# Optimization experiments

Hardware: AMD Instinct MI355X
Metric: run time of the kernel (lower is better)

Reference implementation:

```python
import jax, jax.numpy as jnp
import numpy as np

AX = (-2, -1)
LAMBDA = 0.05
ITERS = 6

# torch fft_2d_img  = fftshift(ifft2(ifftshift(x)))  (used in the FORWARD model)
# torch ifft_2d_img = ifftshift(fft2(fftshift(x)))   (used in the ADJOINT model)

def _fwd_xform(x):
    return jnp.fft.fftshift(jnp.fft.ifft2(jnp.fft.ifftshift(x, axes=AX), axes=AX, norm='ortho'), axes=AX)

def _adj_xform(x):
    return jnp.fft.ifftshift(jnp.fft.fft2(jnp.fft.fftshift(x, axes=AX), axes=AX, norm='ortho'), axes=AX)

def _forward_model(img, S, mask):
    # img [b,t,h,w] -> masked multicoil k-space [b,t,c,h,w]
    return mask * _fwd_xform(S * img[:, :, None])

def _adjoint_model(k, S):
    # k [b,t,c,h,w] -> coil-combined image [b,t,h,w]
    return jnp.sum(jnp.conj(S) * _adj_xform(k), axis=2)

def _system_matrix_R(p, S, L, mask):
    # p [b,sv,h,w]; L [b,t,sv]
    expanded = jnp.einsum('bts,bshw->bthw', L, p)
    combined = _adjoint_model(_forward_model(expanded, S, mask), S)
    out = jnp.einsum('bts,bthw->bshw', jnp.conj(L), combined)
    return out + LAMBDA * p

def _cg_solve(b_vec, S, L, mask):
    z0 = jnp.zeros_like(b_vec)
    rs0 = jnp.vdot(b_vec, b_vec)

    def step(carry, _):
        z, r, p, rs_old, done = carry
        Ap = _system_matrix_R(p, S, L, mask)
        alpha = rs_old / (jnp.vdot(p, Ap) + 1e-20)
        z_n = z + alpha * p
        r_n = r - alpha * Ap
        rs_new = jnp.vdot(r_n, r_n)
        p_n = r_n + (rs_new / (rs_old + 1e-20)) * p
        # replicate torch early-break: freeze state once residual is tiny
        z_o = jnp.where(done, z, z_n)
        r_o = jnp.where(done, r, r_n)
        p_o = jnp.where(done, p, p_n)
        rs_o = jnp.where(done, rs_old, rs_new)
        done_n = done | (jnp.abs(rs_o) < 1e-10)
        return (z_o, r_o, p_o, rs_o, done_n), None

    carry0 = (z0, b_vec, b_vec, rs0, jnp.array(False))
    (z, _, _, _, _), _ = jax.lax.scan(step, carry0, None, length=ITERS)
    return z

def setup_inputs() -> dict:
    key = jax.random.key(0)
    ks = jax.random.split(key, 9)
    b, t, c, h, w, sv = 2, 12, 10, 256, 256, 3
    f32 = jnp.float32
    inp = {
        'k_real': jax.random.normal(ks[0], (b, t, c, h, w), f32),
        'k_imag': jax.random.normal(ks[1], (b, t, c, h, w), f32),
        'mo_real': jax.random.normal(ks[2], (b, sv, h, w), f32),
        'mo_imag': jax.random.normal(ks[3], (b, sv, h, w), f32),
        's_real': jax.random.normal(ks[4], (b, 1, c, h, w), f32),
        's_imag': jax.random.normal(ks[5], (b, 1, c, h, w), f32),
        'tb_real': jax.random.normal(ks[6], (b, t, sv), f32),
        'tb_imag': jax.random.normal(ks[7], (b, t, sv), f32),
        'mask': (jax.random.uniform(ks[8], (b, t, 1, h, w)) < 0.35).astype(f32),
    }
    return inp

def reference(k_real, k_imag, mo_real, mo_imag, s_real, s_imag, tb_real, tb_imag, mask):
    Y = k_real + 1j * k_imag          # [b,t,c,h,w]
    MO = mo_real + 1j * mo_imag       # [b,sv,h,w]
    S = s_real + 1j * s_imag          # [b,1,c,h,w]
    L = tb_real + 1j * tb_imag        # [b,t,sv]
    # b = L^H A^H Y + lambda * model_output
    b_vec = jnp.einsum('bts,bthw->bshw', jnp.conj(L), _adjoint_model(Y, S)) + LAMBDA * MO
    z = _cg_solve(b_vec, S, L, mask)  # [b,sv,h,w] complex
    return jnp.stack([z.real, z.imag], axis=-1)  # [b,sv,h,w,2] float32
```

## Files before the change

kernel.cpp:

```cpp
#include <hip/hip_runtime.h>
#include <math.h>

#define HW 65536
#define LAM 0.05f

struct Scal {
  double pap_re, pap_im, rs_acc, rs_old;
  int done, cnt;
};

__device__ __forceinline__ float2 cadd(float2 a, float2 b){ return make_float2(a.x+b.x, a.y+b.y); }
__device__ __forceinline__ float2 csub(float2 a, float2 b){ return make_float2(a.x-b.x, a.y-b.y); }
__device__ __forceinline__ float2 cmul(float2 a, float2 b){
  return make_float2(a.x*b.x - a.y*b.y, a.x*b.y + a.y*b.x);
}
__device__ __forceinline__ float2 cmulj(float2 a, float2 b){
  return make_float2(a.x*b.x + a.y*b.y, a.x*b.y - a.y*b.x);
}
__device__ __forceinline__ int rev4(int p){
  return ((p&3)<<6) | (((p>>2)&3)<<4) | (((p>>4)&3)<<2) | ((p>>6)&3);
}
__device__ __forceinline__ int swz(int p){ return p ^ (p>>4); }

__device__ __forceinline__ void wave_lds_sync(){
  __builtin_amdgcn_wave_barrier();
  __asm__ __volatile__("s_waitcnt lgkmcnt(0)" ::: "memory");
  __builtin_amdgcn_wave_barrier();
}

template<int SIGN>
__device__ void wave_fft256w(float2* buf, int lane){
#pragma unroll
  for (int st=0; st<4; ++st){
    const int B = 256 >> (2*st);
    const int Q = B >> 2;
    int m   = lane & (Q-1);
    int blk = lane >> (6 - 2*st);
    int p0  = blk*B + m;
    float2 x0 = buf[swz(p0      )];
    float2 x1 = buf[swz(p0 +   Q)];
    float2 x2 = buf[swz(p0 + 2*Q)];
    float2 x3 = buf[swz(p0 + 3*Q)];
    float2 a  = cadd(x0,x2), bm = csub(x0,x2);
    float2 c  = cadd(x1,x3), d  = csub(x1,x3);
    float2 jd = make_float2(-(float)SIGN*d.y, (float)SIGN*d.x);
    float2 y0 = cadd(a,c);
    float2 y2 = csub(a,c);
    float2 y1 = cadd(bm,jd);
    float2 y3 = csub(bm,jd);
    if (st < 3){
      float ang = (float)SIGN * 6.28318530717958647f * (float)m / (float)B;
      float s1, c1;
      __sincosf(ang, &s1, &c1);
      float2 w1 = make_float2(c1, s1);
      float2 w2 = make_float2(c1*c1 - s1*s1, 2.f*c1*s1);
      float2 w3 = cmul(w1, w2);
      y1 = cmul(y1, w1); y2 = cmul(y2, w2); y3 = cmul(y3, w3);
      buf[swz(p0      )] = y0;
      buf[swz(p0 +   Q)] = y1;
      buf[swz(p0 + 2*Q)] = y2;
      buf[swz(p0 + 3*Q)] = y3;
    } else {
      buf[swz(rev4(4*lane+0))] = y0;
      buf[swz(rev4(4*lane+1))] = y1;
      buf[swz(rev4(4*lane+2))] = y2;
      buf[swz(rev4(4*lane+3))] = y3;
    }
    wave_lds_sync();
  }
}

__global__ __launch_bounds__(256) void k_w(const float* __restrict__ mask,
                                           const float* __restrict__ tbr,
                                           const float* __restrict__ tbi,
                                           float2* __restrict__ Wb,
                                           Scal* sc){
  if (blockIdx.x==0 && blockIdx.y==0 && threadIdx.x==0){
    sc->pap_re=0.0; sc->pap_im=0.0; sc->rs_acc=0.0; sc->rs_old=0.0;
    sc->done=0; sc->cnt=0;
  }
  __shared__ float2 wt[9][16][17];
  int tid = threadIdx.x;
  int bx = blockIdx.x;
  int b  = blockIdx.y;
  int u0 = (bx>>4)<<4, v0 = (bx&15)<<4;
  int u_l = tid>>4, v_l = tid&15;
  int pix = (u0+u_l)*256 + (v0+v_l);
  float d0=0,d1=0,d2=0, o01r=0,o01i=0, o02r=0,o02i=0, o12r=0,o12i=0;
#pragma unroll
  for (int t=0;t<12;t++){
    float m = mask[(size_t)(b*12+t)*HW + pix];
    int lb = (b*12+t)*3;
    float l0r = tbr[lb+0], l0i = tbi[lb+0];
    float l1r = tbr[lb+1], l1i = tbi[lb+1];
    float l2r = tbr[lb+2], l2i = tbi[lb+2];
    d0 += m*(l0r*l0r + l0i*l0i);
    d1 += m*(l1r*l1r + l1i*l1i);
    d2 += m*(l2r*l2r + l2i*l2i);
    o01r += m*(l0r*l1r + l0i*l1i); o01i += m*(l0r*l1i - l0i*l1r);
    o02r += m*(l0r*l2r + l0i*l2i); o02i += m*(l0r*l2i - l0i*l2r);
    o12r += m*(l1r*l2r + l1i*l2i); o12i += m*(l1r*l2i - l1i*l2r);
  }
  const float s = 1.0f/65536.0f;
  wt[0][u_l][v_l] = make_float2(d0*s, 0.f);
  wt[1][u_l][v_l] = make_float2(o01r*s,  o01i*s);
  wt[2][u_l][v_l] = make_float2(o02r*s,  o02i*s);
  wt[3][u_l][v_l] = make_float2(o01r*s, -o01i*s);
  wt[4][u_l][v_l] = make_float2(d1*s, 0.f);
  wt[5][u_l][v_l] = make_float2(o12r*s,  o12i*s);
  wt[6][u_l][v_l] = make_float2(o02r*s, -o02i*s);
  wt[7][u_l][v_l] = make_float2(o12r*s, -o12i*s);
  wt[8][u_l][v_l] = make_float2(d2*s, 0.f);
  __syncthreads();
  int u_l2 = tid&15, v_l2 = tid>>4;
#pragma unroll
  for (int k=0;k<9;k++){
    Wb[ ((size_t)(b*9+k)*256 + (v0+v_l2))*256 + (u0+u_l2) ] = wt[k][u_l2][v_l2];
  }
}

__global__ __launch_bounds__(256) void k_yhat(const float* __restrict__ kr,
                                              const float* __restrict__ ki,
                                              const float* __restrict__ tbr,
                                              const float* __restrict__ tbi,
                                              float2* __restrict__ bufA){
  int tid = threadIdx.x;
  int pr  = blockIdx.x*256 + tid;
  int pix = pr*2;
  int c = blockIdx.y, b = blockIdx.z;
  float aer[3]={0,0,0}, aei[3]={0,0,0}, bor[3]={0,0,0}, boi[3]={0,0,0};
#pragma unroll
  for (int t=0;t<12;t++){
    size_t off = ((size_t)((b*12+t)*10+c))*HW + pix;
    float2 yr = *(const float2*)(kr+off);
    float2 yi = *(const float2*)(ki+off);
    int lb = (b*12+t)*3;
#pragma unroll
    for (int s=0;s<3;s++){
      float lr = tbr[lb+s], li = tbi[lb+s];
      aer[s] += lr*yr.x + li*yi.x;  aei[s] += lr*yi.x - li*yr.x;
      bor[s] += lr*yr.y + li*yi.y;  boi[s] += lr*yi.y - li*yr.y;
    }
  }
  float sg0 = (((pix>>8) ^ pix) & 1) ? -1.f : 1.f;
  float s0 = sg0*(1.0f/256.0f), s1 = -s0;
  size_t base = ((size_t)(b*10+c))*3*HW + pix;
#pragma unroll
  for (int s=0;s<3;s++){
    float4 o = make_float4(aer[s]*s0, aei[s]*s0, bor[s]*s1, boi[s]*s1);
    *(float4*)(&bufA[base + (size_t)s*HW]) = o;
  }
}

template<int MODE>
__global__ __launch_bounds__(256) void k_colpass(float2* __restrict__ bufA,
                                                 const float2* __restrict__ Wb){
  __shared__ float2 lb[24*257];
  int tid = threadIdx.x, wave = tid>>6, lane = tid&63;
  int j0 = blockIdx.x*8;
  int c = blockIdx.y, b = blockIdx.z;
  for (int s=0;s<3;s++){
    const float2* src = bufA + ((size_t)(b*30 + c*3 + s))*HW;
#pragma unroll
    for (int it=0; it<8; it++){
      int idx = it*256 + tid;
      int u = idx>>3, col = idx&7;
      lb[(s*8+col)*257 + swz(u)] = src[u*256 + j0 + col];
    }
  }
  __syncthreads();
  if (MODE==0){
    for (int fc=wave; fc<24; fc+=4)
      wave_fft256w<-1>(&lb[fc*257], lane);
  } else {
    for (int fc=wave; fc<24; fc+=4)
      wave_fft256w<1>(&lb[fc*257], lane);
    const float2* Wp = Wb + (size_t)b*9*HW;
#pragma unroll
    for (int cc=0; cc<2; cc++){
      int col = wave + 4*cc;
      int v = j0 + col;
#pragma unroll
      for (int it=0; it<4; it++){
        int u = lane + it*64;
        int su = swz(u);
        float2 x0 = lb[(0*8+col)*257 + su];
        float2 x1 = lb[(1*8+col)*257 + su];
        float2 x2 = lb[(2*8+col)*257 + su];
        size_t wb = (size_t)v*256 + u;
        float2 y0 = cmul(Wp[(size_t)0*HW + wb], x0);
        y0 = cadd(y0, cmul(Wp[(size_t)1*HW + wb], x1));
        y0 = cadd(y0, cmul(Wp[(size_t)2*HW + wb], x2));
        float2 y1 = cmul(Wp[(size_t)3*HW + wb], x0);
        y1 = cadd(y1, cmul(Wp[(size_t)4*HW + wb], x1));
        y1 = cadd(y1, cmul(Wp[(size_t)5*HW + wb], x2));
        float2 y2 = cmul(Wp[(size_t)6*HW + wb], x0);
        y2 = cadd(y2, cmul(Wp[(size_t)7*HW + wb], x1));
        y2 = cadd(y2, cmul(Wp[(size_t)8*HW + wb], x2));
        lb[(0*8+col)*257 + su] = y0;
        lb[(1*8+col)*257 + su] = y1;
        lb[(2*8+col)*257 + su] = y2;
      }
    }
    wave_lds_sync();
    for (int fc=wave; fc<24; fc+=4)
      wave_fft256w<-1>(&lb[fc*257], lane);
  }
  __syncthreads();
  for (int s=0;s<3;s++){
    float2* dst = bufA + ((size_t)(b*30 + c*3 + s))*HW;
#pragma unroll
    for (int it=0; it<8; it++){
      int idx = it*256 + tid;
      int u = idx>>3, col = idx&7;
      dst[u*256 + j0 + col] = lb[(s*8+col)*257 + swz(u)];
    }
  }
}

__global__ __launch_bounds__(256) void k_spfft(const float2* __restrict__ p,
                                               const float* __restrict__ sr_,
                                               const float* __restrict__ si_,
                                               float2* __restrict__ bufA){
  __shared__ float2 lb[30*257];
  int tid = threadIdx.x, wave = tid>>6, lane = tid&63;
  int r = blockIdx.x, b = blockIdx.y;
  int k = tid;
  float2 pv[3];
#pragma unroll
  for (int s=0;s<3;s++)
    pv[s] = p[(size_t)(b*3+s)*HW + (size_t)r*256 + k];
  int sk = swz(k);
#pragma unroll
  for (int c=0;c<10;c++){
    size_t so = (size_t)(b*10+c)*HW + (size_t)r*256 + k;
    float2 sv = make_float2(sr_[so], si_[so]);
#pragma unroll
    for (int s=0;s<3;s++)
      lb[(c*3+s)*257 + sk] = cmul(sv, pv[s]);
  }
  __syncthreads();
  for (int pl=wave; pl<30; pl+=4){
    float2* lw = &lb[pl*257];
    wave_fft256w<1>(lw, lane);
    float2* dst = bufA + (size_t)(b*30+pl)*HW + (size_t)r*256;
#pragma unroll
    for (int q=0;q<4;q++){
      int kk = lane + 64*q;
      dst[kk] = lw[swz(kk)];
    }
  }
}

template<int SETUP>
__global__ __launch_bounds__(256) void k_rowcomb(const float2* __restrict__ bufA,
                                                 const float* __restrict__ sr_,
                                                 const float* __restrict__ si_,
                                                 const float* __restrict__ mor,
                                                 const float* __restrict__ moi,
                                                 const float2* __restrict__ pad,
                                                 float2* __restrict__ out,
                                                 Scal* sc){
  __shared__ float2 lb[30*257];
  __shared__ double sd[4], sd2[4];
  int tid = threadIdx.x, wave = tid>>6, lane = tid&63;
  int r = blockIdx.x, b = blockIdx.y;
  if (!SETUP && r==0 && b==0 && tid==0) sc->rs_acc = 0.0;
  for (int pl=wave; pl<30; pl+=4){
    const float2* src = bufA + (size_t)(b*30+pl)*HW + (size_t)r*256;
    float2* lw = &lb[pl*257];
#pragma unroll
    for (int q=0;q<4;q++){
      int kk = lane + 64*q;
      lw[swz(kk)] = src[kk];
    }
    wave_lds_sync();
    wave_fft256w<-1>(lw, lane);
  }
  __syncthreads();
  int k = tid, sk = swz(k);
  float2 a0 = make_float2(0,0), a1 = make_float2(0,0), a2 = make_float2(0,0);
#pragma unroll
  for (int c=0;c<10;c++){
    size_t so = (size_t)(b*10+c)*HW + (size_t)r*256 + k;
    float2 sv = make_float2(sr_[so], si_[so]);
    a0 = cadd(a0, cmulj(sv, lb[(c*3+0)*257 + sk]));
    a1 = cadd(a1, cmulj(sv, lb[(c*3+1)*257 + sk]));
    a2 = cadd(a2, cmulj(sv, lb[(c*3+2)*257 + sk]));
  }
  float2 accs[3] = {a0, a1, a2};
  double dre = 0.0, dim = 0.0;
#pragma unroll
  for (int s=0;s<3;s++){
    size_t oi = (size_t)(b*3+s)*HW + (size_t)r*256 + k;
    float2 acc = accs[s];
    if (SETUP){
      float sg = ((r ^ k) & 1) ? -1.f : 1.f;
      float sl = sg * LAM;
      acc.x += sl*mor[oi]; acc.y += sl*moi[oi];
      out[oi] = acc;
      dre += (double)acc.x*acc.x + (double)acc.y*acc.y;
    } else {
      float2 av = pad[oi];
      acc.x += LAM*av.x; acc.y += LAM*av.y;
      out[oi] = acc;
      dre += (double)av.x*acc.x + (double)av.y*acc.y;
      dim += (double)av.x*acc.y - (double)av.y*acc.x;
    }
  }
  for (int off=32; off>0; off>>=1){
    dre += __shfl_down(dre, off, 64);
    if (!SETUP) dim += __shfl_down(dim, off, 64);
  }
  if (lane==0){ sd[wave] = dre; sd2[wave] = dim; }
  __syncthreads();
  if (tid==0){
    double tre = sd[0]+sd[1]+sd[2]+sd[3];
    if (SETUP){
      atomicAdd(&sc->rs_acc, tre);
    } else {
      double tim = sd2[0]+sd2[1]+sd2[2]+sd2[3];
      atomicAdd(&sc->pap_re, tre);
      atomicAdd(&sc->pap_im, tim);
    }
  }
}

__global__ __launch_bounds__(256) void k_cginit(const float2* __restrict__ bvec,
                                                float2* __restrict__ z,
                                                float2* __restrict__ r,
                                                float2* __restrict__ p,
                                                Scal* sc){
  int i = blockIdx.x*256 + threadIdx.x;
  float2 bv = bvec[i];
  z[i] = make_float2(0.f,0.f);
  r[i] = bv; p[i] = bv;
  if (i==0){ sc->rs_old = sc->rs_acc; sc->pap_re=0.0; sc->pap_im=0.0; }
}

__global__ __launch_bounds__(256) void k_upzr(float2* __restrict__ z,
                                              float2* __restrict__ r,
                                              const float2* __restrict__ p,
                                              const float2* __restrict__ Ap,
                                              Scal* sc){
  __shared__ double sd[4];
  int tid = threadIdx.x;
  int i = blockIdx.x*256 + tid;
  int done = sc->done;
  double local = 0.0;
  if (!done){
    double dre = sc->pap_re + 1e-20, dim = sc->pap_im;
    double den = dre*dre + dim*dim;
    double rs = sc->rs_old;
    float2 alpha = make_float2((float)( rs*dre/den), (float)(-rs*dim/den));
    float2 pv = p[i], apv = Ap[i];
    float2 zv = cadd(z[i], cmul(alpha, pv));
    float2 rv = csub(r[i], cmul(alpha, apv));
    z[i] = zv; r[i] = rv;
    local = (double)rv.x*rv.x + (double)rv.y*rv.y;
  }
  for (int off=32; off>0; off>>=1) local += __shfl_down(local, off, 64);
  if ((tid&63)==0) sd[tid>>6] = local;
  __syncthreads();
  if (tid==0 && !done){
    atomicAdd(&sc->rs_acc, sd[0]+sd[1]+sd[2]+sd[3]);
  }
}

__global__ __launch_bounds__(256) void k_upp(float2* __restrict__ p,
                                             const float2* __restrict__ r,
                                             Scal* sc){
  __shared__ int amLast;
  int tid = threadIdx.x;
  int i = blockIdx.x*256 + tid;
  int done = sc->done;
  if (!done){
    float beta = (float)(sc->rs_acc / (sc->rs_old + 1e-20));
    float2 pv = p[i];
    p[i] = make_float2(r[i].x + beta*pv.x, r[i].y + beta*pv.y);
  }
  if (tid==0){
    int prev = atomicAdd(&sc->cnt, 1);
    amLast = (prev == (int)gridDim.x - 1);
  }
  __syncthreads();
  if (tid==0 && amLast){
    sc->cnt = 0;
    if (!sc->done){
      sc->rs_old = sc->rs_acc;
      if (fabs(sc->rs_old) < 1e-10) sc->done = 1;
    }
    sc->pap_re = 0.0; sc->pap_im = 0.0;
  }
}

__global__ __launch_bounds__(256) void k_out(const float2* __restrict__ z,
                                             float* __restrict__ out){
  int i = blockIdx.x*256 + threadIdx.x;
  int pix = i & (HW-1);
  float sgn = (((pix>>8)^pix)&1) ? -1.f : 1.f;
  float2 zv = z[i];
  out[2*i]   = sgn*zv.x;
  out[2*i+1] = sgn*zv.y;
}

extern "C" void kernel_launch(void* const* d_in, const int* in_sizes, int n_in,
                              void* d_out, int out_size, void* d_ws, size_t ws_size,
                              hipStream_t stream){
  const float* kr   = (const float*)d_in[0];
  const float* ki   = (const float*)d_in[1];
  const float* mor  = (const float*)d_in[2];
  const float* moi  = (const float*)d_in[3];
  const float* sr   = (const float*)d_in[4];
  const float* si   = (const float*)d_in[5];
  const float* tbr  = (const float*)d_in[6];
  const float* tbi  = (const float*)d_in[7];
  const float* mask = (const float*)d_in[8];
  float* out = (float*)d_out;

  float2* ws   = (float2*)d_ws;
  float2* bufA = ws;
  float2* Wb   = ws + 3932160;
  float2* bvec = ws + 5111808;
  float2* z    = ws + 5505024;
  float2* r    = ws + 5898240;
  float2* p    = ws + 6291456;
  float2* Ap   = ws + 6684672;
  Scal*   sc   = (Scal*)(ws + 7077888);

  k_w<<<dim3(256,2),dim3(256),0,stream>>>(mask, tbr, tbi, Wb, sc);
  k_yhat<<<dim3(128,10,2),dim3(256),0,stream>>>(kr, ki, tbr, tbi, bufA);
  k_colpass<0><<<dim3(32,10,2),dim3(256),0,stream>>>(bufA, Wb);
  k_rowcomb<1><<<dim3(256,2),dim3(256),0,stream>>>(bufA, sr, si, mor, moi,
                                                   (const float2*)0, bvec, sc);
  k_cginit<<<dim3(1536),dim3(256),0,stream>>>(bvec, z, r, p, sc);
  for (int it=0; it<6; ++it){
    k_spfft<<<dim3(256,2),dim3(256),0,stream>>>(p, sr, si, bufA);
    k_colpass<1><<<dim3(32,10,2),dim3(256),0,stream>>>(bufA, Wb);
    k_rowcomb<0><<<dim3(256,2),dim3(256),0,stream>>>(bufA, sr, si,
                                                     (const float*)0,
                                                     (const float*)0,
                                                     p, Ap, sc);
    k_upzr<<<dim3(1536),dim3(256),0,stream>>>(z, r, p, Ap, sc);
    k_upp<<<dim3(1536),dim3(256),0,stream>>>(p, r, sc);
  }
  k_out<<<dim3(1536),dim3(256),0,stream>>>(z, out);
}
```

Measured before the change: 871.9 us.

## Fuse p-update into spfft, pair FFTs per wave, vectorize global accesses

Removes the separate k_upp kernel by computing p = r + beta*p inside k_spfft and moving the scalar bookkeeping (rs_old/done/reset) into its last-block atomic epilogue. Each wave now runs two 256-point FFTs interleaved, to raise ILP and halve sync overhead. Global loads and stores in yhat, colpass, spfft and rowcomb are widened to float4. This saves one launch and a full pass over p and r per CG iteration, but moves the rs_acc reset and p-update ordering into a different kernel, which risks subtle correctness issues. The paired FFTs also raise register pressure.

```diff
diff --git a/kernel.cpp b/kernel.cpp
--- a/kernel.cpp
+++ b/kernel.cpp
@@ -29,7 +29,16 @@
 }
 
 template<int SIGN>
-__device__ void wave_fft256w(float2* buf, int lane){
+__device__ __forceinline__ void bfly4(float2 x0, float2 x1, float2 x2, float2 x3,
+                                      float2& y0, float2& y1, float2& y2, float2& y3){
+  float2 a  = cadd(x0,x2), bm = csub(x0,x2);
+  float2 c  = cadd(x1,x3), d  = csub(x1,x3);
+  float2 jd = make_float2(-(float)SIGN*d.y, (float)SIGN*d.x);
+  y0 = cadd(a,c); y2 = csub(a,c); y1 = cadd(bm,jd); y3 = csub(bm,jd);
+}
+
+template<int SIGN>
+__device__ void wave_fft256w_x2(float2* bA, float2* bB, int lane){
 #pragma unroll
   for (int st=0; st<4; ++st){
     const int B = 256 >> (2*st);
@@ -37,17 +46,12 @@
     int m   = lane & (Q-1);
     int blk = lane >> (6 - 2*st);
     int p0  = blk*B + m;
-    float2 x0 = buf[swz(p0      )];
-    float2 x1 = buf[swz(p0 +   Q)];
-    float2 x2 = buf[swz(p0 + 2*Q)];
-    float2 x3 = buf[swz(p0 + 3*Q)];
-    float2 a  = cadd(x0,x2), bm = csub(x0,x2);
-    float2 c  = cadd(x1,x3), d  = csub(x1,x3);
-    float2 jd = make_float2(-(float)SIGN*d.y, (float)SIGN*d.x);
-    float2 y0 = cadd(a,c);
-    float2 y2 = csub(a,c);
-    float2 y1 = cadd(bm,jd);
-    float2 y3 = csub(bm,jd);
+    int i0 = swz(p0), i1 = swz(p0+Q), i2 = swz(p0+2*Q), i3 = swz(p0+3*Q);
+    float2 xA0=bA[i0], xA1=bA[i1], xA2=bA[i2], xA3=bA[i3];
+    float2 xB0=bB[i0], xB1=bB[i1], xB2=bB[i2], xB3=bB[i3];
+    float2 yA0,yA1,yA2,yA3, yB0,yB1,yB2,yB3;
+    bfly4<SIGN>(xA0,xA1,xA2,xA3, yA0,yA1,yA2,yA3);
+    bfly4<SIGN>(xB0,xB1,xB2,xB3, yB0,yB1,yB2,yB3);
     if (st < 3){
       float ang = (float)SIGN * 6.28318530717958647f * (float)m / (float)B;
       float s1, c1;
@@ -55,16 +59,13 @@
       float2 w1 = make_float2(c1, s1);
       float2 w2 = make_float2(c1*c1 - s1*s1, 2.f*c1*s1);
       float2 w3 = cmul(w1, w2);
-      y1 = cmul(y1, w1); y2 = cmul(y2, w2); y3 = cmul(y3, w3);
-      buf[swz(p0      )] = y0;
-      buf[swz(p0 +   Q)] = y1;
-      buf[swz(p0 + 2*Q)] = y2;
-      buf[swz(p0 + 3*Q)] = y3;
+      bA[i0]=yA0; bA[i1]=cmul(yA1,w1); bA[i2]=cmul(yA2,w2); bA[i3]=cmul(yA3,w3);
+      bB[i0]=yB0; bB[i1]=cmul(yB1,w1); bB[i2]=cmul(yB2,w2); bB[i3]=cmul(yB3,w3);
     } else {
-      buf[swz(rev4(4*lane+0))] = y0;
-      buf[swz(rev4(4*lane+1))] = y1;
-      buf[swz(rev4(4*lane+2))] = y2;
-      buf[swz(rev4(4*lane+3))] = y3;
+      int r0=swz(rev4(4*lane+0)), r1=swz(rev4(4*lane+1));
+      int r2=swz(rev4(4*lane+2)), r3=swz(rev4(4*lane+3));
+      bA[r0]=yA0; bA[r1]=yA1; bA[r2]=yA2; bA[r3]=yA3;
+      bB[r0]=yB0; bB[r1]=yB1; bB[r2]=yB2; bB[r3]=yB3;
     }
     wave_lds_sync();
   }
@@ -125,30 +126,40 @@
                                               const float* __restrict__ tbi,
                                               float2* __restrict__ bufA){
   int tid = threadIdx.x;
-  int pr  = blockIdx.x*256 + tid;
-  int pix = pr*2;
+  int pix = (blockIdx.x*256 + tid)*4;
   int c = blockIdx.y, b = blockIdx.z;
-  float aer[3]={0,0,0}, aei[3]={0,0,0}, bor[3]={0,0,0}, boi[3]={0,0,0};
+  float ar[3][4], ai[3][4];
+#pragma unroll
+  for (int s=0;s<3;s++)
+#pragma unroll
+    for (int j=0;j<4;j++){ ar[s][j]=0.f; ai[s][j]=0.f; }
 #pragma unroll
   for (int t=0;t<12;t++){
     size_t off = ((size_t)((b*12+t)*10+c))*HW + pix;
-    float2 yr = *(const float2*)(kr+off);
-    float2 yi = *(const float2*)(ki+off);
+    float4 yr = *(const float4*)(kr+off);
+    float4 yi = *(const float4*)(ki+off);
+    float yrv[4] = {yr.x, yr.y, yr.z, yr.w};
+    float yiv[4] = {yi.x, yi.y, yi.z, yi.w};
     int lb = (b*12+t)*3;
 #pragma unroll
     for (int s=0;s<3;s++){
       float lr = tbr[lb+s], li = tbi[lb+s];
-      aer[s] += lr*yr.x + li*yi.x;  aei[s] += lr*yi.x - li*yr.x;
-      bor[s] += lr*yr.y + li*yi.y;  boi[s] += lr*yi.y - li*yr.y;
+#pragma unroll
+      for (int j=0;j<4;j++){
+        ar[s][j] += lr*yrv[j] + li*yiv[j];
+        ai[s][j] += lr*yiv[j] - li*yrv[j];
+      }
     }
   }
   float sg0 = (((pix>>8) ^ pix) & 1) ? -1.f : 1.f;
-  float s0 = sg0*(1.0f/256.0f), s1 = -s0;
+  float sg[4] = { sg0*(1.f/256.f), -sg0*(1.f/256.f), sg0*(1.f/256.f), -sg0*(1.f/256.f) };
   size_t base = ((size_t)(b*10+c))*3*HW + pix;
 #pragma unroll
   for (int s=0;s<3;s++){
-    float4 o = make_float4(aer[s]*s0, aei[s]*s0, bor[s]*s1, boi[s]*s1);
-    *(float4*)(&bufA[base + (size_t)s*HW]) = o;
+    float4 o0 = make_float4(ar[s][0]*sg[0], ai[s][0]*sg[0], ar[s][1]*sg[1], ai[s][1]*sg[1]);
+    float4 o1 = make_float4(ar[s][2]*sg[2], ai[s][2]*sg[2], ar[s][3]*sg[3], ai[s][3]*sg[3]);
+    *(float4*)(&bufA[base + (size_t)s*HW])     = o0;
+    *(float4*)(&bufA[base + (size_t)s*HW + 2]) = o1;
   }
 }
 
@@ -162,23 +173,25 @@
   for (int s=0;s<3;s++){
     const float2* src = bufA + ((size_t)(b*30 + c*3 + s))*HW;
 #pragma unroll
-    for (int it=0; it<8; it++){
+    for (int it=0; it<4; it++){
       int idx = it*256 + tid;
-      int u = idx>>3, col = idx&7;
-      lb[(s*8+col)*257 + swz(u)] = src[u*256 + j0 + col];
+      int u = idx>>2, cp = idx&3;
+      float4 v = *(const float4*)(src + u*256 + j0 + 2*cp);
+      lb[(s*8+2*cp  )*257 + swz(u)] = make_float2(v.x, v.y);
+      lb[(s*8+2*cp+1)*257 + swz(u)] = make_float2(v.z, v.w);
     }
   }
   __syncthreads();
   if (MODE==0){
-    for (int fc=wave; fc<24; fc+=4)
-      wave_fft256w<-1>(&lb[fc*257], lane);
+    for (int fc=wave*2; fc<24; fc+=8)
+      wave_fft256w_x2<-1>(&lb[fc*257], &lb[(fc+1)*257], lane);
   } else {
-    for (int fc=wave; fc<24; fc+=4)
-      wave_fft256w<1>(&lb[fc*257], lane);
+    for (int fc=wave*2; fc<24; fc+=8)
+      wave_fft256w_x2<1>(&lb[fc*257], &lb[(fc+1)*257], lane);
     const float2* Wp = Wb + (size_t)b*9*HW;
 #pragma unroll
     for (int cc=0; cc<2; cc++){
-      int col = wave + 4*cc;
+      int col = wave*2 + cc;
       int v = j0 + col;
 #pragma unroll
       for (int it=0; it<4; it++){
@@ -203,33 +216,48 @@
       }
     }
     wave_lds_sync();
-    for (int fc=wave; fc<24; fc+=4)
-      wave_fft256w<-1>(&lb[fc*257], lane);
+    for (int fc=wave*2; fc<24; fc+=8)
+      wave_fft256w_x2<-1>(&lb[fc*257], &lb[(fc+1)*257], lane);
   }
   __syncthreads();
   for (int s=0;s<3;s++){
     float2* dst = bufA + ((size_t)(b*30 + c*3 + s))*HW;
 #pragma unroll
-    for (int it=0; it<8; it++){
+    for (int it=0; it<4; it++){
       int idx = it*256 + tid;
-      int u = idx>>3, col = idx&7;
-      dst[u*256 + j0 + col] = lb[(s*8+col)*257 + swz(u)];
-    }
-  }
-}
-
-__global__ __launch_bounds__(256) void k_spfft(const float2* __restrict__ p,
+      int u = idx>>2, cp = idx&3;
+      float2 e0 = lb[(s*8+2*cp  )*257 + swz(u)];
+      float2 e1 = lb[(s*8+2*cp+1)*257 + swz(u)];
+      *(float4*)(dst + u*256 + j0 + 2*cp) = make_float4(e0.x, e0.y, e1.x, e1.y);
+    }
+  }
+}
+
+__global__ __launch_bounds__(256) void k_spfft(float2* __restrict__ p,
+                                               const float2* __restrict__ rvec,
                                                const float* __restrict__ sr_,
                                                const float* __restrict__ si_,
-                                               float2* __restrict__ bufA){
+                                               float2* __restrict__ bufA,
+                                               Scal* sc, int first){
   __shared__ float2 lb[30*257];
   int tid = threadIdx.x, wave = tid>>6, lane = tid&63;
   int r = blockIdx.x, b = blockIdx.y;
   int k = tid;
+  int done = sc->done;
+  float beta = 0.f;
+  if (!first) beta = (float)(sc->rs_acc / (sc->rs_old + 1e-20));
   float2 pv[3];
 #pragma unroll
-  for (int s=0;s<3;s++)
-    pv[s] = p[(size_t)(b*3+s)*HW + (size_t)r*256 + k];
+  for (int s=0;s<3;s++){
+    size_t oi = (size_t)(b*3+s)*HW + (size_t)r*256 + k;
+    if (!first && !done){
+      float2 po = p[oi], rv = rvec[oi];
+      float2 pn = make_float2(rv.x + beta*po.x, rv.y + beta*po.y);
+      p[oi] = pn; pv[s] = pn;
+    } else {
+      pv[s] = p[oi];
+    }
+  }
   int sk = swz(k);
 #pragma unroll
   for (int c=0;c<10;c++){
@@ -240,14 +268,31 @@
       lb[(c*3+s)*257 + sk] = cmul(sv, pv[s]);
   }
   __syncthreads();
-  for (int pl=wave; pl<30; pl+=4){
-    float2* lw = &lb[pl*257];
-    wave_fft256w<1>(lw, lane);
-    float2* dst = bufA + (size_t)(b*30+pl)*HW + (size_t)r*256;
-#pragma unroll
-    for (int q=0;q<4;q++){
-      int kk = lane + 64*q;
-      dst[kk] = lw[swz(kk)];
+  for (int pl=wave*2; pl<30; pl+=8){
+    float2* lwA = &lb[pl*257];
+    float2* lwB = &lb[(pl+1)*257];
+    wave_fft256w_x2<1>(lwA, lwB, lane);
+    float2* dA = bufA + (size_t)(b*30+pl)*HW + (size_t)r*256;
+    float2* dB = bufA + (size_t)(b*30+pl+1)*HW + (size_t)r*256;
+#pragma unroll
+    for (int q=0;q<2;q++){
+      int j = lane + 64*q;
+      float2 a0 = lwA[swz(2*j)], a1 = lwA[swz(2*j+1)];
+      float2 b0 = lwB[swz(2*j)], b1 = lwB[swz(2*j+1)];
+      *(float4*)(dA + 2*j) = make_float4(a0.x,a0.y,a1.x,a1.y);
+      *(float4*)(dB + 2*j) = make_float4(b0.x,b0.y,b1.x,b1.y);
+    }
+  }
+  if (tid==0){
+    int total = (int)(gridDim.x*gridDim.y);
+    int prev = atomicAdd(&sc->cnt, 1);
+    if (prev == total-1){
+      sc->cnt = 0;
+      if (!first && !sc->done){
+        sc->rs_old = sc->rs_acc;
+        if (fabs(sc->rs_old) < 1e-10) sc->done = 1;
+      }
+      sc->pap_re = 0.0; sc->pap_im = 0.0; sc->rs_acc = 0.0;
     }
   }
 }
@@ -265,17 +310,21 @@
   __shared__ double sd[4], sd2[4];
   int tid = threadIdx.x, wave = tid>>6, lane = tid&63;
   int r = blockIdx.x, b = blockIdx.y;
-  if (!SETUP && r==0 && b==0 && tid==0) sc->rs_acc = 0.0;
-  for (int pl=wave; pl<30; pl+=4){
-    const float2* src = bufA + (size_t)(b*30+pl)*HW + (size_t)r*256;
-    float2* lw = &lb[pl*257];
-#pragma unroll
-    for (int q=0;q<4;q++){
-      int kk = lane + 64*q;
-      lw[swz(kk)] = src[kk];
+  for (int pl=wave*2; pl<30; pl+=8){
+    const float2* sA = bufA + (size_t)(b*30+pl)*HW + (size_t)r*256;
+    const float2* sB = bufA + (size_t)(b*30+pl+1)*HW + (size_t)r*256;
+    float2* lwA = &lb[pl*257];
+    float2* lwB = &lb[(pl+1)*257];
+#pragma unroll
+    for (int q=0;q<2;q++){
+      int j = lane + 64*q;
+      float4 va = *(const float4*)(sA + 2*j);
+      float4 vb = *(const float4*)(sB + 2*j);
+      lwA[swz(2*j)] = make_float2(va.x,va.y); lwA[swz(2*j+1)] = make_float2(va.z,va.w);
+      lwB[swz(2*j)] = make_float2(vb.x,vb.y); lwB[swz(2*j+1)] = make_float2(vb.z,vb.w);
     }
     wave_lds_sync();
-    wave_fft256w<-1>(lw, lane);
+    wave_fft256w_x2<-1>(lwA, lwB, lane);
   }
   __syncthreads();
   int k = tid, sk = swz(k);
@@ -367,33 +416,6 @@
   }
 }
 
-__global__ __launch_bounds__(256) void k_upp(float2* __restrict__ p,
-                                             const float2* __restrict__ r,
-                                             Scal* sc){
-  __shared__ int amLast;
-  int tid = threadIdx.x;
-  int i = blockIdx.x*256 + tid;
-  int done = sc->done;
-  if (!done){
-    float beta = (float)(sc->rs_acc / (sc->rs_old + 1e-20));
-    float2 pv = p[i];
-    p[i] = make_float2(r[i].x + beta*pv.x, r[i].y + beta*pv.y);
-  }
-  if (tid==0){
-    int prev = atomicAdd(&sc->cnt, 1);
-    amLast = (prev == (int)gridDim.x - 1);
-  }
-  __syncthreads();
-  if (tid==0 && amLast){
-    sc->cnt = 0;
-    if (!sc->done){
-      sc->rs_old = sc->rs_acc;
-      if (fabs(sc->rs_old) < 1e-10) sc->done = 1;
-    }
-    sc->pap_re = 0.0; sc->pap_im = 0.0;
-  }
-}
-
 __global__ __launch_bounds__(256) void k_out(const float2* __restrict__ z,
                                              float* __restrict__ out){
   int i = blockIdx.x*256 + threadIdx.x;
@@ -429,20 +451,19 @@
   Scal*   sc   = (Scal*)(ws + 7077888);
 
   k_w<<<dim3(256,2),dim3(256),0,stream>>>(mask, tbr, tbi, Wb, sc);
-  k_yhat<<<dim3(128,10,2),dim3(256),0,stream>>>(kr, ki, tbr, tbi, bufA);
+  k_yhat<<<dim3(64,10,2),dim3(256),0,stream>>>(kr, ki, tbr, tbi, bufA);
   k_colpass<0><<<dim3(32,10,2),dim3(256),0,stream>>>(bufA, Wb);
   k_rowcomb<1><<<dim3(256,2),dim3(256),0,stream>>>(bufA, sr, si, mor, moi,
                                                    (const float2*)0, bvec, sc);
   k_cginit<<<dim3(1536),dim3(256),0,stream>>>(bvec, z, r, p, sc);
   for (int it=0; it<6; ++it){
-    k_spfft<<<dim3(256,2),dim3(256),0,stream>>>(p, sr, si, bufA);
+    k_spfft<<<dim3(256,2),dim3(256),0,stream>>>(p, r, sr, si, bufA, sc, it==0 ? 1 : 0);
     k_colpass<1><<<dim3(32,10,2),dim3(256),0,stream>>>(bufA, Wb);
     k_rowcomb<0><<<dim3(256,2),dim3(256),0,stream>>>(bufA, sr, si,
                                                      (const float*)0,
                                                      (const float*)0,
                                                      p, Ap, sc);
     k_upzr<<<dim3(1536),dim3(256),0,stream>>>(z, r, p, Ap, sc);
-    k_upp<<<dim3(1536),dim3(256),0,stream>>>(p, r, sc);
   }
   k_out<<<dim3(1536),dim3(256),0,stream>>>(z, out);
 }
```

New measurement: 761.3 us. 12.7% less time.
